# Optimization experiments

Measured on AMD Instinct MI355X. Metric: run time of the kernel, lower is better.

## Reference

```python
import jax, jax.numpy as jnp
import numpy as np

B, S, D, H = 2, 2048, 1024, 16
HD = D // H  # head_dim = 64


def setup_inputs() -> dict:
    key = jax.random.key(0)
    ks = jax.random.split(key, 11)
    sc = 1.0 / np.sqrt(D)
    inp = {
        "query": jax.random.normal(ks[0], (B, S, D), jnp.float32),
        "key_": jax.random.normal(ks[1], (B, S, D), jnp.float32),
        "value": jax.random.normal(ks[2], (B, S, D), jnp.float32),
        "Wq": jax.random.normal(ks[3], (D, D), jnp.float32) * sc,
        "bq": jnp.zeros((D,), jnp.float32),
        "Wk": jax.random.normal(ks[4], (D, D), jnp.float32) * sc,
        "bk": jnp.zeros((D,), jnp.float32),
        "Wv": jax.random.normal(ks[5], (D, D), jnp.float32) * sc,
        "bv": jnp.zeros((D,), jnp.float32),
        "Wo": jax.random.normal(ks[6], (D, D), jnp.float32) * sc,
        "bo": jnp.zeros((D,), jnp.float32),
    }
    return inp


def _split_heads(x):
    # [B,S,D] -> [B,H,S,HD]
    return x.reshape(B, -1, H, HD).transpose(0, 2, 1, 3)


def reference(query, key_, value, Wq, bq, Wk, bk, Wv, bv, Wo, bo):
    q = _split_heads(query @ Wq.T + bq)
    k = _split_heads(key_ @ Wk.T + bk)
    v = _split_heads(value @ Wv.T + bv)
    scores = jnp.einsum("bhqd,bhkd->bhqk", q, k) / jnp.sqrt(jnp.float32(HD))
    attn = jax.nn.softmax(scores, axis=-1)  # dropout is identity in eval
    out = jnp.einsum("bhqk,bhkd->bhqd", attn, v)
    out = out.transpose(0, 2, 1, 3).reshape(B, -1, D)
    return out @ Wo.T + bo
```

## Files before the change

### kernel.cpp

```cpp
#include <hip/hip_runtime.h>
#include <hip/hip_bf16.h>
#include <stdint.h>

#define B_  2
#define S_  2048
#define D_  1024
#define H_  16
#define HD_ 64
#define M_  (B_*S_)

typedef __bf16 bf16x8 __attribute__((ext_vector_type(8)));
typedef __bf16 bf16x4 __attribute__((ext_vector_type(4)));
typedef short  s16x4  __attribute__((ext_vector_type(4)));
typedef float  f32x4  __attribute__((ext_vector_type(4)));
typedef unsigned int u32x4 __attribute__((ext_vector_type(4)));
typedef unsigned int u32x2 __attribute__((ext_vector_type(2)));
typedef unsigned short ushort_t;
typedef ushort_t u16x8 __attribute__((ext_vector_type(8)));

#define LOG2E 1.44269504088896f

#if __has_builtin(__builtin_amdgcn_exp2f)
#define EXP2(x) __builtin_amdgcn_exp2f(x)
#else
#define EXP2(x) exp2f(x)
#endif

__device__ __forceinline__ ushort_t f2bf(float f) {
    return __builtin_bit_cast(ushort_t, (__bf16)f);
}
__device__ __forceinline__ bf16x8 load_frag(const ushort_t* p) {
    u32x4 r = *reinterpret_cast<const u32x4*>(p);
    return __builtin_bit_cast(bf16x8, r);
}
__device__ __forceinline__ bf16x8 lds_frag(const ushort_t* p) {
    u32x4 r = *reinterpret_cast<const u32x4*>(p);
    return __builtin_bit_cast(bf16x8, r);
}
__device__ __forceinline__ bf16x4 lds_frag4(const ushort_t* p) {
    u32x2 r = *reinterpret_cast<const u32x2*>(p);
    return __builtin_bit_cast(bf16x4, r);
}
__device__ __forceinline__ void gld_lds16(const ushort_t* g, ushort_t* l) {
    __builtin_amdgcn_global_load_lds(
        (const __attribute__((address_space(1))) void*)g,
        (__attribute__((address_space(3))) void*)l, 16, 0, 0);
}

__device__ __forceinline__ f32x4 mfma16_bf16(bf16x4 a, bf16x4 b, f32x4 c) {
#if __has_builtin(__builtin_amdgcn_mfma_f32_16x16x16_bf16)
    return __builtin_amdgcn_mfma_f32_16x16x16_bf16(a, b, c, 0, 0, 0);
#elif __has_builtin(__builtin_amdgcn_mfma_f32_16x16x16bf16_1k)
    return __builtin_amdgcn_mfma_f32_16x16x16bf16_1k(
        __builtin_bit_cast(s16x4, a), __builtin_bit_cast(s16x4, b), c, 0, 0, 0);
#else
    f32x4 d;
    asm("v_mfma_f32_16x16x16_bf16 %0, %1, %2, %3"
        : "=v"(d) : "v"(a), "v"(b), "v"(c));
    return d;
#endif
}

__device__ __forceinline__ void cvt_body(const float* __restrict__ in,
                                         ushort_t* __restrict__ out, int i) {
    f32x4 v0 = *reinterpret_cast<const f32x4*>(in + i);
    f32x4 v1 = *reinterpret_cast<const f32x4*>(in + i + 4);
    u16x8 o;
#pragma unroll
    for (int j = 0; j < 4; ++j) { o[j] = f2bf(v0[j]); o[4 + j] = f2bf(v1[j]); }
    *reinterpret_cast<u16x8*>(out + i) = o;
}

__global__ __launch_bounds__(256) void cvt_all_kernel(
    const float* q, const float* k, const float* v,
    const float* fwq, const float* fwk, const float* fwv, const float* fwo,
    ushort_t* oq, ushort_t* ok, ushort_t* ov,
    ushort_t* owq, ushort_t* owk, ushort_t* owv, ushort_t* owo)
{
    const size_t T = (size_t)M_ * D_;
    const size_t U = (size_t)D_ * D_;
    const size_t idx = ((size_t)blockIdx.x * 256 + threadIdx.x) * 8;
    const float* in; ushort_t* out; size_t off;
    if (idx < 3 * T) {
        const size_t w = idx >> 22; off = idx & (T - 1);
        in  = (w == 0) ? q  : (w == 1) ? k  : v;
        out = (w == 0) ? oq : (w == 1) ? ok : ov;
    } else {
        const size_t r = idx - 3 * T;
        const size_t w = r >> 20; off = r & (U - 1);
        in  = (w == 0) ? fwq : (w == 1) ? fwk : (w == 2) ? fwv : fwo;
        out = (w == 0) ? owq : (w == 1) ? owk : (w == 2) ? owv : owo;
    }
    cvt_body(in, out, (int)off);
}

__device__ __forceinline__ void gemm_body(const ushort_t* __restrict__ X,
                                          const ushort_t* __restrict__ W,
                                          const float* __restrict__ bias,
                                          void* __restrict__ out, int mode)
{
    __shared__ ushort_t lA[2][128 * 32];
    __shared__ ushort_t lB[2][128 * 32];

    const int tid  = threadIdx.x;
    const int lane = tid & 63;
    const int wv   = tid >> 6;
    const int m0   = blockIdx.x * 128;
    const int n0   = blockIdx.y * 128;
    const int wr   = (wv >> 1) * 64;
    const int wc   = (wv & 1) * 64;
    const int l15  = lane & 15;
    const int lg   = lane >> 4;

    f32x4 acc[4][4];
#pragma unroll
    for (int i = 0; i < 4; ++i)
#pragma unroll
        for (int j = 0; j < 4; ++j) acc[i][j] = (f32x4){0.f, 0.f, 0.f, 0.f};

    const int srow = lane >> 2;
    const int sk   = (lane & 3) * 8;
    const int c0   = wv * 2, c1 = wv * 2 + 1;
    const size_t arow0 = (size_t)(m0 + c0 * 16 + srow) * D_ + sk;
    const size_t arow1 = (size_t)(m0 + c1 * 16 + srow) * D_ + sk;
    const size_t brow0 = (size_t)(n0 + c0 * 16 + srow) * D_ + sk;
    const size_t brow1 = (size_t)(n0 + c1 * 16 + srow) * D_ + sk;

    gld_lds16(X + arow0, &lA[0][c0 * 512]);
    gld_lds16(X + arow1, &lA[0][c1 * 512]);
    gld_lds16(W + brow0, &lB[0][c0 * 512]);
    gld_lds16(W + brow1, &lB[0][c1 * 512]);

    const int NKT = D_ / 32;
    for (int kt = 0; kt < NKT; ++kt) {
        const int cur = kt & 1;
        __builtin_amdgcn_s_barrier();
        if (kt + 1 < NKT) {
            const int k0 = (kt + 1) * 32;
            gld_lds16(X + arow0 + k0, &lA[cur ^ 1][c0 * 512]);
            gld_lds16(X + arow1 + k0, &lA[cur ^ 1][c1 * 512]);
            gld_lds16(W + brow0 + k0, &lB[cur ^ 1][c0 * 512]);
            gld_lds16(W + brow1 + k0, &lB[cur ^ 1][c1 * 512]);
            asm volatile("s_waitcnt vmcnt(4)" ::: "memory");
        } else {
            asm volatile("s_waitcnt vmcnt(0)" ::: "memory");
        }
        __builtin_amdgcn_s_barrier();

        bf16x8 a[4], b[4];
#pragma unroll
        for (int i = 0; i < 4; ++i)
            a[i] = lds_frag(&lA[cur][(wr + i * 16 + l15) * 32 + lg * 8]);
#pragma unroll
        for (int j = 0; j < 4; ++j)
            b[j] = lds_frag(&lB[cur][(wc + j * 16 + l15) * 32 + lg * 8]);
#pragma unroll
        for (int i = 0; i < 4; ++i)
#pragma unroll
            for (int j = 0; j < 4; ++j)
                acc[i][j] = __builtin_amdgcn_mfma_f32_16x16x32_bf16(a[i], b[j], acc[i][j], 0, 0, 0);
    }

#pragma unroll
    for (int i = 0; i < 4; ++i) {
#pragma unroll
        for (int j = 0; j < 4; ++j) {
            const int gcol = n0 + wc + j * 16 + l15;
            const float bv = bias[gcol];
#pragma unroll
            for (int r = 0; r < 4; ++r) {
                const int grow = m0 + wr + i * 16 + lg * 4 + r;
                float v = acc[i][j][r] + bv;
                if (mode == 0) v *= 0.125f * LOG2E;
                if (mode == 3) {
                    ((float*)out)[(size_t)grow * D_ + gcol] = v;
                } else {
                    const int b = grow >> 11, s = grow & (S_ - 1);
                    const int h = gcol >> 6,  hd = gcol & 63;
                    size_t addr;
                    if (mode == 2) addr = ((size_t)(b * H_ + h) * HD_ + hd) * S_ + s;
                    else           addr = ((size_t)(b * H_ + h) * S_ + s) * HD_ + hd;
                    ((ushort_t*)out)[addr] = f2bf(v);
                }
            }
        }
    }
}

__global__ __launch_bounds__(256) void qkv_kernel(
    const ushort_t* q_in, const ushort_t* k_in, const ushort_t* v_in,
    const ushort_t* Wq, const ushort_t* Wk, const ushort_t* Wv,
    const float* bq, const float* bk, const float* bv,
    ushort_t* qo, ushort_t* ko, ushort_t* vo)
{
    const int z = blockIdx.z;
    const ushort_t* X  = (z == 0) ? q_in : (z == 1) ? k_in : v_in;
    const ushort_t* W  = (z == 0) ? Wq   : (z == 1) ? Wk   : Wv;
    const float*    bs = (z == 0) ? bq   : (z == 1) ? bk   : bv;
    ushort_t*       o  = (z == 0) ? qo   : (z == 1) ? ko   : vo;
    gemm_body(X, W, bs, o, (z == 2) ? 2 : z);
}

__global__ __launch_bounds__(256) void oproj_kernel(
    const ushort_t* X, const ushort_t* W, const float* bias, float* out)
{
    gemm_body(X, W, bias, out, 3);
}

#define KVB 64
#define NT  (S_ / KVB)
#define SM_K0 0
#define SM_K1 4096
#define SM_V0 8192
#define SM_V1 12288
#define SM_TOT 17920

__global__ __launch_bounds__(512, 4) void attn_kernel(
    const ushort_t* __restrict__ Q, const ushort_t* __restrict__ K,
    const ushort_t* __restrict__ VT, ushort_t* __restrict__ O)
{
    __shared__ ushort_t smem[SM_TOT];

    const int lane = threadIdx.x & 63;
    const int wv   = threadIdx.x >> 6;
    const int wq   = wv & 3;
    const int wkv  = wv >> 2;
    const int bh   = blockIdx.x;
    const int qb   = blockIdx.y;
    const int qbase = qb * 128 + wq * 32;
    const int l15  = lane & 15;
    const int lg   = lane >> 4;

    const ushort_t* Qp = Q  + (size_t)bh * S_ * HD_;
    const ushort_t* Kp = K  + (size_t)bh * S_ * HD_;
    const ushort_t* Vp = VT + (size_t)bh * HD_ * S_;

    const int kr = threadIdx.x >> 3;
    const int kc = ((threadIdx.x & 7) ^ (kr & 7)) * 8;
    const int koff = threadIdx.x * 8;

    auto stage = [&](int tile, ushort_t* kdst, ushort_t* vdst) {
        gld_lds16(Kp + (size_t)(tile * KVB + kr) * HD_ + kc, kdst + koff);
        gld_lds16(Vp + (size_t)kr * S_ + tile * KVB + kc,    vdst + koff);
    };

    int offk[2][2];
#pragma unroll
    for (int j = 0; j < 2; ++j)
#pragma unroll
        for (int c = 0; c < 2; ++c)
            offk[j][c] = (wkv * 32 + j * 16 + l15) * 64 +
                         ((c * 32 + lg * 8) ^ ((l15 & 7) << 3));
    int offv[4][2];
#pragma unroll
    for (int dt = 0; dt < 4; ++dt)
#pragma unroll
        for (int j = 0; j < 2; ++j)
            offv[dt][j] = (dt * 16 + l15) * 64 +
                          (((wkv * 4 + j * 2 + (lg >> 1)) ^ (l15 & 7)) << 3) +
                          (lg & 1) * 4;

    bf16x8 aq[2][2];
#pragma unroll
    for (int qh = 0; qh < 2; ++qh)
#pragma unroll
        for (int c = 0; c < 2; ++c)
            aq[c][qh] = load_frag(Qp + (size_t)(qbase + qh * 16 + l15) * HD_ + c * 32 + lg * 8);

    f32x4 accO[4][2];
#pragma unroll
    for (int dt = 0; dt < 4; ++dt)
#pragma unroll
        for (int qh = 0; qh < 2; ++qh) accO[dt][qh] = (f32x4){0.f, 0.f, 0.f, 0.f};
    float lrun0 = 0.f, lrun1 = 0.f;

    stage(0, &smem[SM_K0], &smem[SM_V0]);

    for (int t = 0; t < NT; ++t) {
        const int cur = t & 1;
        const ushort_t* kb = cur ? &smem[SM_K1] : &smem[SM_K0];
        const ushort_t* vb = cur ? &smem[SM_V1] : &smem[SM_V0];

        __builtin_amdgcn_s_barrier();
        if (t + 1 < NT) {
            stage(t + 1, cur ? &smem[SM_K0] : &smem[SM_K1],
                          cur ? &smem[SM_V0] : &smem[SM_V1]);
            asm volatile("s_waitcnt vmcnt(2)" ::: "memory");
        } else {
            asm volatile("s_waitcnt vmcnt(0)" ::: "memory");
        }
        __builtin_amdgcn_s_barrier();
        __builtin_amdgcn_sched_barrier(0);

        f32x4 st[2][2];
#pragma unroll
        for (int j = 0; j < 2; ++j)
#pragma unroll
            for (int qh = 0; qh < 2; ++qh) st[j][qh] = (f32x4){0.f, 0.f, 0.f, 0.f};
        __builtin_amdgcn_s_setprio(1);
#pragma unroll
        for (int j = 0; j < 2; ++j) {
            bf16x8 k0 = lds_frag(&kb[offk[j][0]]);
            bf16x8 k1 = lds_frag(&kb[offk[j][1]]);
            st[j][0] = __builtin_amdgcn_mfma_f32_16x16x32_bf16(k0, aq[0][0], st[j][0], 0, 0, 0);
            st[j][0] = __builtin_amdgcn_mfma_f32_16x16x32_bf16(k1, aq[1][0], st[j][0], 0, 0, 0);
            st[j][1] = __builtin_amdgcn_mfma_f32_16x16x32_bf16(k0, aq[0][1], st[j][1], 0, 0, 0);
            st[j][1] = __builtin_amdgcn_mfma_f32_16x16x32_bf16(k1, aq[1][1], st[j][1], 0, 0, 0);
        }
        __builtin_amdgcn_s_setprio(0);

        bf16x4 pb[2][2];
#pragma unroll
        for (int qh = 0; qh < 2; ++qh) {
#pragma unroll
            for (int j = 0; j < 2; ++j) {
                float p0 = EXP2(st[j][qh][0]);
                float p1 = EXP2(st[j][qh][1]);
                float p2 = EXP2(st[j][qh][2]);
                float p3 = EXP2(st[j][qh][3]);
                u32x2 w;
                w[0] = (unsigned)f2bf(p0) | ((unsigned)f2bf(p1) << 16);
                w[1] = (unsigned)f2bf(p2) | ((unsigned)f2bf(p3) << 16);
                pb[j][qh] = __builtin_bit_cast(bf16x4, w);
                const float s = (p0 + p1) + (p2 + p3);
                if (qh == 0) lrun0 += s; else lrun1 += s;
            }
        }

        __builtin_amdgcn_s_setprio(1);
#pragma unroll
        for (int dt = 0; dt < 4; ++dt) {
#pragma unroll
            for (int j = 0; j < 2; ++j) {
                bf16x4 vf = lds_frag4(&vb[offv[dt][j]]);
                accO[dt][0] = mfma16_bf16(vf, pb[j][0], accO[dt][0]);
                accO[dt][1] = mfma16_bf16(vf, pb[j][1], accO[dt][1]);
            }
        }
        __builtin_amdgcn_s_setprio(0);
    }

    lrun0 += __shfl_xor(lrun0, 16);
    lrun0 += __shfl_xor(lrun0, 32);
    lrun1 += __shfl_xor(lrun1, 16);
    lrun1 += __shfl_xor(lrun1, 32);

    __syncthreads();
    float* cbuf = (float*)smem;

    if (wkv == 1) {
#pragma unroll
        for (int qh = 0; qh < 2; ++qh) {
            const int rowq = (wq * 2 + qh) * 16 + l15;
#pragma unroll
            for (int dt = 0; dt < 4; ++dt)
                *reinterpret_cast<f32x4*>(&cbuf[rowq * 68 + dt * 16 + lg * 4]) = accO[dt][qh];
        }
        if (lane < 16) {
            cbuf[128 * 68 + (wq * 2 + 0) * 16 + lane] = lrun0;
            cbuf[128 * 68 + (wq * 2 + 1) * 16 + lane] = lrun1;
        }
    }
    __syncthreads();

    if (wkv == 0) {
        const int b = bh >> 4, h = bh & 15;
#pragma unroll
        for (int qh = 0; qh < 2; ++qh) {
            const int rowq = (wq * 2 + qh) * 16 + l15;
            const float lsum = (qh == 0 ? lrun0 : lrun1) + cbuf[128 * 68 + rowq];
            const float inv = 1.0f / lsum;
            const size_t rowbase =
                (size_t)(b * S_ + qbase + qh * 16 + l15) * D_ + h * 64;
#pragma unroll
            for (int dt = 0; dt < 4; ++dt) {
                f32x4 part = *reinterpret_cast<f32x4*>(&cbuf[rowq * 68 + dt * 16 + lg * 4]);
                f32x4 tot  = accO[dt][qh] + part;
                u32x2 w;
                w[0] = (unsigned)f2bf(tot[0] * inv) | ((unsigned)f2bf(tot[1] * inv) << 16);
                w[1] = (unsigned)f2bf(tot[2] * inv) | ((unsigned)f2bf(tot[3] * inv) << 16);
                *reinterpret_cast<u32x2*>(&O[rowbase + dt * 16 + lg * 4]) = w;
            }
        }
    }
}

extern "C" void kernel_launch(void* const* d_in, const int* in_sizes, int n_in,
                              void* d_out, int out_size, void* d_ws, size_t ws_size,
                              hipStream_t stream)
{
    const float* query = (const float*)d_in[0];
    const float* key_  = (const float*)d_in[1];
    const float* value = (const float*)d_in[2];
    const float* Wq    = (const float*)d_in[3];
    const float* bq    = (const float*)d_in[4];
    const float* Wk    = (const float*)d_in[5];
    const float* bk    = (const float*)d_in[6];
    const float* Wv    = (const float*)d_in[7];
    const float* bv    = (const float*)d_in[8];
    const float* Wo    = (const float*)d_in[9];
    const float* bo    = (const float*)d_in[10];

    ushort_t* ws   = (ushort_t*)d_ws;
    const size_t T = (size_t)M_ * D_;
    const size_t U = (size_t)D_ * D_;
    ushort_t* xq  = ws;
    ushort_t* xk  = xq + T;
    ushort_t* xv  = xk + T;
    ushort_t* wq  = xv + T;
    ushort_t* wk  = wq + U;
    ushort_t* wv  = wk + U;
    ushort_t* wo  = wv + U;
    ushort_t* qws  = wo + U;
    ushort_t* kws  = qws + T;
    ushort_t* vtws = kws + T;
    ushort_t* aows = vtws + T;

    const int cvt_blocks = (int)((3 * T + 4 * U) / (256 * 8));
    cvt_all_kernel<<<cvt_blocks, 256, 0, stream>>>(
        query, key_, value, Wq, Wk, Wv, Wo,
        xq, xk, xv, wq, wk, wv, wo);

    qkv_kernel<<<dim3(32, 8, 3), 256, 0, stream>>>(
        xq, xk, xv, wq, wk, wv, bq, bk, bv, qws, kws, vtws);

    attn_kernel<<<dim3(32, 16), 512, 0, stream>>>(qws, kws, vtws, aows);

    oproj_kernel<<<dim3(32, 8, 1), 256, 0, stream>>>(
        aows, wo, bo, (float*)d_out);
}
```

Measured before the change: 133.4 us.

## Swizzle GEMM LDS tiles and drop double buffering in projection GEMM

The projection GEMM now XOR-swizzles the 16-byte k-chunks in LDS, on both the global-to-LDS store side and the fragment read side, to avoid LDS bank conflicts when reading MFMA fragments. It also replaces the two-stage double-buffered LDS pipeline with a single buffer and two __syncthreads per k-step, which halves LDS use. Global loads are no longer overlapped with MFMA work inside a block, so latency hiding now depends on occupancy. The __syncthreads is assumed to wait for the async global-to-LDS loads.

```diff
diff --git a/kernel.cpp b/kernel.cpp
--- a/kernel.cpp
+++ b/kernel.cpp
@@ -99,8 +99,8 @@
                                           const float* __restrict__ bias,
                                           void* __restrict__ out, int mode)
 {
-    __shared__ ushort_t lA[2][128 * 32];
-    __shared__ ushort_t lB[2][128 * 32];
+    __shared__ ushort_t lA[128 * 32];
+    __shared__ ushort_t lB[128 * 32];
 
     const int tid  = threadIdx.x;
     const int lane = tid & 63;
@@ -119,46 +119,36 @@
         for (int j = 0; j < 4; ++j) acc[i][j] = (f32x4){0.f, 0.f, 0.f, 0.f};
 
     const int srow = lane >> 2;
-    const int sk   = (lane & 3) * 8;
+    const int skc  = ((lane & 3) ^ ((srow >> 1) & 3)) * 8;
     const int c0   = wv * 2, c1 = wv * 2 + 1;
-    const size_t arow0 = (size_t)(m0 + c0 * 16 + srow) * D_ + sk;
-    const size_t arow1 = (size_t)(m0 + c1 * 16 + srow) * D_ + sk;
-    const size_t brow0 = (size_t)(n0 + c0 * 16 + srow) * D_ + sk;
-    const size_t brow1 = (size_t)(n0 + c1 * 16 + srow) * D_ + sk;
-
-    gld_lds16(X + arow0, &lA[0][c0 * 512]);
-    gld_lds16(X + arow1, &lA[0][c1 * 512]);
-    gld_lds16(W + brow0, &lB[0][c0 * 512]);
-    gld_lds16(W + brow1, &lB[0][c1 * 512]);
-
-    const int NKT = D_ / 32;
-    for (int kt = 0; kt < NKT; ++kt) {
-        const int cur = kt & 1;
-        __builtin_amdgcn_s_barrier();
-        if (kt + 1 < NKT) {
-            const int k0 = (kt + 1) * 32;
-            gld_lds16(X + arow0 + k0, &lA[cur ^ 1][c0 * 512]);
-            gld_lds16(X + arow1 + k0, &lA[cur ^ 1][c1 * 512]);
-            gld_lds16(W + brow0 + k0, &lB[cur ^ 1][c0 * 512]);
-            gld_lds16(W + brow1 + k0, &lB[cur ^ 1][c1 * 512]);
-            asm volatile("s_waitcnt vmcnt(4)" ::: "memory");
-        } else {
-            asm volatile("s_waitcnt vmcnt(0)" ::: "memory");
-        }
-        __builtin_amdgcn_s_barrier();
+    const size_t arow0 = (size_t)(m0 + c0 * 16 + srow) * D_ + skc;
+    const size_t arow1 = (size_t)(m0 + c1 * 16 + srow) * D_ + skc;
+    const size_t brow0 = (size_t)(n0 + c0 * 16 + srow) * D_ + skc;
+    const size_t brow1 = (size_t)(n0 + c1 * 16 + srow) * D_ + skc;
+
+    const int rchunk = (lg ^ ((l15 >> 1) & 3)) * 8;
+
+    for (int kt = 0; kt < D_ / 32; ++kt) {
+        const int k0 = kt * 32;
+        gld_lds16(X + arow0 + k0, &lA[c0 * 512]);
+        gld_lds16(X + arow1 + k0, &lA[c1 * 512]);
+        gld_lds16(W + brow0 + k0, &lB[c0 * 512]);
+        gld_lds16(W + brow1 + k0, &lB[c1 * 512]);
+        __syncthreads();
 
         bf16x8 a[4], b[4];
 #pragma unroll
         for (int i = 0; i < 4; ++i)
-            a[i] = lds_frag(&lA[cur][(wr + i * 16 + l15) * 32 + lg * 8]);
+            a[i] = lds_frag(&lA[(wr + i * 16 + l15) * 32 + rchunk]);
 #pragma unroll
         for (int j = 0; j < 4; ++j)
-            b[j] = lds_frag(&lB[cur][(wc + j * 16 + l15) * 32 + lg * 8]);
+            b[j] = lds_frag(&lB[(wc + j * 16 + l15) * 32 + rchunk]);
 #pragma unroll
         for (int i = 0; i < 4; ++i)
 #pragma unroll
             for (int j = 0; j < 4; ++j)
                 acc[i][j] = __builtin_amdgcn_mfma_f32_16x16x32_bf16(a[i], b[j], acc[i][j], 0, 0, 0);
+        __syncthreads();
     }
 
 #pragma unroll
```

New measurement: 124.3 us (median of 2 runs). 1.07x faster.
